# Kernel optimization log

Measured on AMD Instinct MI355X. Metric: run time of the kernel, lower is better.

Reference implementation:

```python
import jax, jax.numpy as jnp
import numpy as np

EPS = 1e-5  # torch BatchNorm1d default eps


def _bn(y2d, g, b):
    # BatchNorm1d in training mode: biased batch stats over axis 0
    m = y2d.mean(axis=0)
    v = y2d.var(axis=0)
    return (y2d - m) * jax.lax.rsqrt(v + EPS) * g + b


def setup_inputs() -> dict:
    key = jax.random.key(0)
    ks = jax.random.split(key, 18)
    S, B, D, H, O = 1000, 64, 440, 512, 1000
    u = lambda k, shape, n: jax.random.uniform(k, shape, jnp.float32, -1.0 / np.sqrt(n), 1.0 / np.sqrt(n))
    fin = np.sqrt(0.01 / (H + O))
    return {
        "x": jax.random.normal(ks[0], (S, B, D), jnp.float32),
        "Wh": u(ks[1], (H, D), D),
        "Wz": u(ks[2], (H, D), D),
        "Wr": u(ks[3], (H, D), D),
        "Uh": u(ks[4], (H, H), H),
        "Uz": u(ks[5], (H, H), H),
        "Ur": u(ks[6], (H, H), H),
        "gh": 1.0 + 0.1 * jax.random.normal(ks[7], (H,), jnp.float32),
        "bh": 0.1 * jax.random.normal(ks[8], (H,), jnp.float32),
        "gz": 1.0 + 0.1 * jax.random.normal(ks[9], (H,), jnp.float32),
        "bz": 0.1 * jax.random.normal(ks[10], (H,), jnp.float32),
        "gr": 1.0 + 0.1 * jax.random.normal(ks[11], (H,), jnp.float32),
        "br": 0.1 * jax.random.normal(ks[12], (H,), jnp.float32),
        "Wf": jax.random.uniform(ks[13], (O, H), jnp.float32, -fin, fin),
        "gf": 1.0 + 0.1 * jax.random.normal(ks[14], (O,), jnp.float32),
        "bf": 0.1 * jax.random.normal(ks[15], (O,), jnp.float32),
    }


def reference(x, Wh, Wz, Wr, Uh, Uz, Ur, gh, bh, gz, bz, gr, br, Wf, gf, bf):
    S, B, D = x.shape
    H = Wh.shape[0]
    xf = x.reshape(S * B, D)
    # gate input projections (no bias; BN in train mode over flattened (S*B, H))
    wh = _bn(xf @ Wh.T, gh, bh).reshape(S, B, H)
    wz = _bn(xf @ Wz.T, gz, bz).reshape(S, B, H)
    wr = _bn(xf @ Wr.T, gr, br).reshape(S, B, H)

    def step(ht, gates):
        whk, wzk, wrk = gates
        zt = jax.nn.sigmoid(wzk + ht @ Uz.T)
        rt = jax.nn.sigmoid(wrk + ht @ Ur.T)
        hcand = jnp.tanh(whk + (rt * ht) @ Uh.T)  # drop_mask==1 (gru_drop=0.0)
        ht = zt * ht + (1.0 - zt) * hcand
        return ht, ht

    h0 = jnp.zeros((B, H), x.dtype)
    _, h = jax.lax.scan(step, h0, (wh, wz, wr))  # h: (S, B, H)

    ws = _bn(h.reshape(S * B, H) @ Wf.T, gf, bf)
    return jax.nn.log_softmax(ws, axis=1)
```

## Files before the change

### kernel.cpp

```cpp
#include <hip/hip_runtime.h>
#include <cstdint>

typedef unsigned short u16;
typedef unsigned long long u64;
typedef __attribute__((ext_vector_type(8))) short bf16x8;
typedef __attribute__((ext_vector_type(4))) float f32x4;

#define S_LEN 1000
#define NWG   32

#define OFF_HALL   0ull
#define SZ_HALL    (1001ull*64*512*2)
#define OFF_WCAT   (OFF_HALL + SZ_HALL)
#define SZ_WCAT    (1536ull*448*2)
#define OFF_WFB    (OFF_WCAT + SZ_WCAT)
#define SZ_WFB     (1024ull*512*2)
#define OFF_RH     (OFF_WFB + SZ_WFB)
#define SZ_RH      (64ull*512*2)
#define OFF_GSUM   (OFF_RH + SZ_RH)
#define OFF_GSQ    (OFF_GSUM + 1536*4)
#define OFF_AALL   (OFF_GSQ  + 1536*4)
#define OFF_CALL   (OFF_AALL + 1536*4)
#define OFF_SSUM   (OFF_CALL + 1536*4)
#define OFF_SSQ    (OFF_SSUM + 1024*4)
#define OFF_AF     (OFF_SSQ  + 1024*4)
#define OFF_CF     (OFF_AF   + 1024*4)
#define OFF_FLAGS  (OFF_CF   + 1024*4)
#define STATS_ZERO_BYTES (OFF_FLAGS + 2048 - OFF_SSUM)

__device__ __forceinline__ float bf2f(u16 u) {
  union { unsigned u; float f; } v; v.u = ((unsigned)u) << 16; return v.f;
}
__device__ __forceinline__ u16 f2bf(float f) {
  union { float f; unsigned u; } v; v.f = f;
  unsigned r = (v.u + 0x7fffu + ((v.u >> 16) & 1u)) >> 16;
  return (u16)r;
}
__device__ __forceinline__ float sigm(float x) { return 1.f / (1.f + __expf(-x)); }
__device__ __forceinline__ float tanh_(float x) {
  float e = __expf(-2.f * fabsf(x));
  float r = (1.f - e) / (1.f + e);
  return x >= 0.f ? r : -r;
}

__device__ __forceinline__ u64 ld8(const u16* p) {
  return __hip_atomic_load((const u64*)p, __ATOMIC_RELAXED, __HIP_MEMORY_SCOPE_AGENT);
}
__device__ __forceinline__ void st4(u16* p, unsigned v) {
  __hip_atomic_store((unsigned*)p, v, __ATOMIC_RELAXED, __HIP_MEMORY_SCOPE_AGENT);
}
union Frag { u64 q[2]; bf16x8 v; };

__device__ __forceinline__ void stage16(const u16* g, u16* l) {
  __builtin_amdgcn_global_load_lds((const __attribute__((address_space(1))) unsigned int*)(g),
                                   (__attribute__((address_space(3))) unsigned int*)(l), 16, 0, 0);
}

__global__ void cvt_pad(const float* __restrict__ src, u16* __restrict__ dst, int incols, int outcols) {
  int r = blockIdx.x, ci = threadIdx.x;
  float v = (ci < incols) ? src[(size_t)r * incols + ci] : 0.f;
  dst[(size_t)r * outcols + ci] = f2bf(v);
}
__global__ void cvt_wf(const float* __restrict__ src, u16* __restrict__ dst) {
  int r = blockIdx.x, ci = threadIdx.x;
  float v = (r < 1000) ? src[(size_t)r * 512 + ci] : 0.f;
  dst[(size_t)r * 512 + ci] = f2bf(v);
}

template<int MODE>
__global__ __launch_bounds__(256, 1) void gemm_bt(const u16* __restrict__ A, const u16* __restrict__ B,
                                                  void* __restrict__ Cout, int K, int ldc, int nlimit) {
  __shared__ __align__(16) u16 smem[16 * 512];
  const int bm = blockIdx.x * 128;
  const int bn = blockIdx.y * 128;
  const int tid = threadIdx.x;
  const int w = tid >> 6;
  const int lane = tid & 63;
  const int r = lane & 15;
  const int q = lane >> 4;
  const int wm = w & 1, wn = w >> 1;

  f32x4 acc[4][4];
#pragma unroll
  for (int i = 0; i < 4; ++i)
#pragma unroll
    for (int j = 0; j < 4; ++j) acc[i][j] = (f32x4){0.f, 0.f, 0.f, 0.f};

  const u16* gA0 = A + (size_t)(bm + w * 16 + r) * K + q * 8;
  const u16* gA1 = A + (size_t)(bm + (w + 4) * 16 + r) * K + q * 8;
  const u16* gB0 = B + (size_t)(bn + w * 16 + r) * K + q * 8;
  const u16* gB1 = B + (size_t)(bn + (w + 4) * 16 + r) * K + q * 8;
  u16* As = smem;
  u16* Bs = smem + 8 * 512;

  for (int k0 = 0; k0 < K; k0 += 32) {
    stage16(gA0 + k0, As + w * 512);
    stage16(gA1 + k0, As + (w + 4) * 512);
    stage16(gB0 + k0, Bs + w * 512);
    stage16(gB1 + k0, Bs + (w + 4) * 512);
    __syncthreads();
    bf16x8 af[4], bf_[4];
#pragma unroll
    for (int mi = 0; mi < 4; ++mi) af[mi] = *(const bf16x8*)(As + (wm * 4 + mi) * 512 + lane * 8);
#pragma unroll
    for (int ni = 0; ni < 4; ++ni) bf_[ni] = *(const bf16x8*)(Bs + (wn * 4 + ni) * 512 + lane * 8);
#pragma unroll
    for (int mi = 0; mi < 4; ++mi)
#pragma unroll
      for (int ni = 0; ni < 4; ++ni)
        acc[mi][ni] = __builtin_amdgcn_mfma_f32_16x16x32_bf16(af[mi], bf_[ni], acc[mi][ni], 0, 0, 0);
    __syncthreads();
  }
  const int row0 = bm + wm * 64;
  const int col0 = bn + wn * 64;
#pragma unroll
  for (int mi = 0; mi < 4; ++mi)
#pragma unroll
    for (int ni = 0; ni < 4; ++ni) {
      int cc = col0 + ni * 16 + r;
      int rr = row0 + mi * 16 + q * 4;
      if (MODE == 1) {
#pragma unroll
        for (int i = 0; i < 4; ++i)
          if (cc < nlimit) ((float*)Cout)[(size_t)(rr + i) * ldc + cc] = acc[mi][ni][i];
      } else {
        u64 pk = (u64)f2bf(acc[mi][ni][0]) | ((u64)f2bf(acc[mi][ni][1]) << 16) |
                 ((u64)f2bf(acc[mi][ni][2]) << 32) | ((u64)f2bf(acc[mi][ni][3]) << 48);
        *(u64*)((u16*)Cout + (size_t)cc * ldc + rr) = pk;
      }
    }
}

__global__ __launch_bounds__(256, 1) void rowstats(const u16* __restrict__ G,
                                                   float* __restrict__ sum, float* __restrict__ sumsq) {
  const int n = blockIdx.x;
  const u16* row = G + (size_t)n * 64000;
  float s = 0.f, ss = 0.f;
  for (int idx = threadIdx.x * 8; idx < 64000; idx += 2048) {
    union { bf16x8 v; u16 e[8]; } u;
    u.v = *(const bf16x8*)(row + idx);
#pragma unroll
    for (int e = 0; e < 8; ++e) { float f = bf2f(u.e[e]); s += f; ss += f * f; }
  }
#pragma unroll
  for (int o = 32; o > 0; o >>= 1) { s += __shfl_xor(s, o); ss += __shfl_xor(ss, o); }
  __shared__ float ls[4], lss[4];
  if ((threadIdx.x & 63) == 0) { ls[threadIdx.x >> 6] = s; lss[threadIdx.x >> 6] = ss; }
  __syncthreads();
  if (threadIdx.x == 0) {
    sum[n]   = ls[0] + ls[1] + ls[2] + ls[3];
    sumsq[n] = lss[0] + lss[1] + lss[2] + lss[3];
  }
}

__global__ __launch_bounds__(256, 1) void colstats_f32(const float* __restrict__ X, int ld, int ncols,
                                                       float* __restrict__ sum, float* __restrict__ sumsq) {
  const int col = blockIdx.x * 128 + (threadIdx.x & 127);
  const int half = threadIdx.x >> 7;
  const int r0 = blockIdx.y * 2000;
  float s = 0.f, ss = 0.f;
  if (col < ncols) {
    for (int rr = r0 + half; rr < r0 + 2000; rr += 2) {
      float v = X[(size_t)rr * ld + col]; s += v; ss += v * v;
    }
  }
  __shared__ float ls[128], lss[128];
  if (half) { ls[threadIdx.x & 127] = s; lss[threadIdx.x & 127] = ss; }
  __syncthreads();
  if (!half && col < ncols) {
    s += ls[threadIdx.x]; ss += lss[threadIdx.x];
    atomicAdd(&sum[col], s); atomicAdd(&sumsq[col], ss);
  }
}

__global__ void fin_gate(const float* __restrict__ sum, const float* __restrict__ sq,
                         const float* gh, const float* bh, const float* gz, const float* bz,
                         const float* gr, const float* br, float* __restrict__ a, float* __restrict__ c) {
  int j = blockIdx.x * 256 + threadIdx.x;
  if (j >= 1536) return;
  float m = sum[j] * (1.f / 64000.f);
  float v = sq[j] * (1.f / 64000.f) - m * m;
  int seg = j >> 9, jj = j & 511;
  float gg = seg == 0 ? gh[jj] : seg == 1 ? gz[jj] : gr[jj];
  float bb = seg == 0 ? bh[jj] : seg == 1 ? bz[jj] : br[jj];
  float aa = gg * rsqrtf(v + 1e-5f);
  a[j] = aa; c[j] = bb - m * aa;
}

__global__ void fin_score(const float* __restrict__ sum, const float* __restrict__ sq,
                          const float* __restrict__ gfp, const float* __restrict__ bfp,
                          float* __restrict__ a, float* __restrict__ c) {
  int j = blockIdx.x * 256 + threadIdx.x;
  if (j >= 1000) return;
  float m = sum[j] * (1.f / 64000.f);
  float v = sq[j] * (1.f / 64000.f) - m * m;
  float aa = gfp[j] * rsqrtf(v + 1e-5f);
  a[j] = aa; c[j] = bfp[j] - m * aa;
}

__device__ __forceinline__ void publish_and_wait(unsigned* flags, int g, unsigned val) {
  asm volatile("s_waitcnt vmcnt(0)" ::: "memory");
  __syncthreads();
  if (threadIdx.x == 0)
    __hip_atomic_store(&flags[g * 16], val, __ATOMIC_RELAXED, __HIP_MEMORY_SCOPE_AGENT);
  if (threadIdx.x < 64) {
    const int l = threadIdx.x;
    for (;;) {
      unsigned v = (l < NWG) ? __hip_atomic_load(&flags[l * 16], __ATOMIC_RELAXED, __HIP_MEMORY_SCOPE_AGENT)
                             : val;
      if (__all(v >= val)) break;
      __builtin_amdgcn_s_sleep(1);
    }
  }
  __syncthreads();
  asm volatile("" ::: "memory");
}

__global__ __launch_bounds__(256, 1) void scan_kernel(
    const u16* __restrict__ gatesT,
    const float* __restrict__ Uz, const float* __restrict__ Ur, const float* __restrict__ Uh,
    const float* __restrict__ acoef, const float* __restrict__ ccoef,
    u16* __restrict__ hall,
    u16* __restrict__ rh,
    unsigned* __restrict__ flags) {
  __shared__ __align__(16) u16 Us[3][16][520];
  __shared__ float co[6][16];
  const int g = blockIdx.x;
  const int j0 = g * 16;
  const int tid = threadIdx.x;
  const int w = tid >> 6;
  const int lane = tid & 63;
  const int r = lane & 15;
  const int q = lane >> 4;

  for (int idx = tid; idx < 3 * 16 * 512; idx += 256) {
    int u = idx >> 13;
    int rem = idx & 8191;
    int j = rem >> 9;
    int k = rem & 511;
    const float* U = (u == 0) ? Uz : (u == 1) ? Ur : Uh;
    Us[u][j][k] = f2bf(U[(size_t)(j0 + j) * 512 + k]);
  }
  if (tid < 16) {
    co[0][tid] = acoef[512 + j0 + tid];  co[1][tid] = ccoef[512 + j0 + tid];
    co[2][tid] = acoef[1024 + j0 + tid]; co[3][tid] = ccoef[1024 + j0 + tid];
    co[4][tid] = acoef[j0 + tid];        co[5][tid] = ccoef[j0 + tid];
  }
  __syncthreads();
  const float az = co[0][r], cz = co[1][r], ar = co[2][r], cr = co[3][r];
  const float ah = co[4][r], ch = co[5][r];

  const u16* gRowH = gatesT + (size_t)(j0 + r) * 64000;
  const u16* gRowZ = gatesT + (size_t)(512 + j0 + r) * 64000;
  const u16* gRowR = gatesT + (size_t)(1024 + j0 + r) * 64000;

  float hp[4] = {0.f, 0.f, 0.f, 0.f};

  for (int t = 1; t <= S_LEN; ++t) {
    const int ct = (t - 1) * 64 + w * 16 + q * 4;
    const u64 wzq = *(const u64*)(gRowZ + ct);
    const u64 wrq = *(const u64*)(gRowR + ct);
    const u64 whq = *(const u64*)(gRowH + ct);

    const u16* hprev = hall + (size_t)(t - 1) * (64 * 512);
    f32x4 accz = {0.f, 0.f, 0.f, 0.f}, accr = {0.f, 0.f, 0.f, 0.f};
    const u16* arow = hprev + (size_t)(w * 16 + r) * 512 + q * 8;
#pragma unroll
    for (int ks = 0; ks < 16; ++ks) {
      Frag a; a.q[0] = ld8(arow + ks * 32); a.q[1] = ld8(arow + ks * 32 + 4);
      bf16x8 bz = *(const bf16x8*)(&Us[0][r][ks * 32 + q * 8]);
      bf16x8 br2 = *(const bf16x8*)(&Us[1][r][ks * 32 + q * 8]);
      accz = __builtin_amdgcn_mfma_f32_16x16x32_bf16(a.v, bz, accz, 0, 0, 0);
      accr = __builtin_amdgcn_mfma_f32_16x16x32_bf16(a.v, br2, accr, 0, 0, 0);
    }
    float zv[4];
#pragma unroll
    for (int i = 0; i < 4; ++i) {
      float wz = bf2f((u16)(wzq >> (16 * i)));
      float wr = bf2f((u16)(wrq >> (16 * i)));
      zv[i] = sigm(accz[i] + wz * az + cz);
      float rv = sigm(accr[i] + wr * ar + cr);
      u16 rhb = f2bf(rv * hp[i]);
      float partner = __shfl_xor(bf2f(rhb), 1);
      if ((r & 1) == 0)
        st4(rh + (size_t)(w * 16 + q * 4 + i) * 512 + j0 + r,
            (unsigned)rhb | ((unsigned)f2bf(partner) << 16));
    }
    publish_and_wait(flags, g, 2 * t - 1);

    f32x4 acch = {0.f, 0.f, 0.f, 0.f};
    const u16* rrow = rh + (size_t)(w * 16 + r) * 512 + q * 8;
#pragma unroll
    for (int ks = 0; ks < 16; ++ks) {
      Frag a; a.q[0] = ld8(rrow + ks * 32); a.q[1] = ld8(rrow + ks * 32 + 4);
      bf16x8 bh = *(const bf16x8*)(&Us[2][r][ks * 32 + q * 8]);
      acch = __builtin_amdgcn_mfma_f32_16x16x32_bf16(a.v, bh, acch, 0, 0, 0);
    }
    u16* hnew = hall + (size_t)t * (64 * 512);
#pragma unroll
    for (int i = 0; i < 4; ++i) {
      float wh = bf2f((u16)(whq >> (16 * i)));
      float hc = tanh_(acch[i] + wh * ah + ch);
      float hn = zv[i] * hp[i] + (1.f - zv[i]) * hc;
      u16 hb = f2bf(hn);
      hp[i] = bf2f(hb);
      float partner = __shfl_xor(hp[i], 1);
      if ((r & 1) == 0)
        st4(hnew + (size_t)(w * 16 + q * 4 + i) * 512 + j0 + r,
            (unsigned)hb | ((unsigned)f2bf(partner) << 16));
    }
    publish_and_wait(flags, g, 2 * t);
  }
}

__global__ __launch_bounds__(256, 1) void logsoftmax_k(float* __restrict__ S,
                                                       const float* __restrict__ a, const float* __restrict__ c) {
  __shared__ float as_[1000], cs_[1000];
  for (int i = threadIdx.x; i < 1000; i += 256) { as_[i] = a[i]; cs_[i] = c[i]; }
  __syncthreads();
  const int w = threadIdx.x >> 6, lane = threadIdx.x & 63;
  for (int it = 0; it < 4; ++it) {
    const int row = blockIdx.x * 16 + it * 4 + w;
    float* Srow = S + (size_t)row * 1000;
    float tv[16];
    float mx = -3.0e38f;
#pragma unroll
    for (int qq = 0; qq < 16; ++qq) {
      int j = lane + qq * 64;
      float v = -3.0e38f;
      if (j < 1000) v = as_[j] * Srow[j] + cs_[j];
      tv[qq] = v;
      mx = fmaxf(mx, v);
    }
#pragma unroll
    for (int o = 32; o > 0; o >>= 1) mx = fmaxf(mx, __shfl_xor(mx, o));
    float sm = 0.f;
#pragma unroll
    for (int qq = 0; qq < 16; ++qq) sm += __expf(tv[qq] - mx);
#pragma unroll
    for (int o = 32; o > 0; o >>= 1) sm += __shfl_xor(sm, o);
    float lse = mx + __logf(sm);
#pragma unroll
    for (int qq = 0; qq < 16; ++qq) {
      int j = lane + qq * 64;
      if (j < 1000) Srow[j] = tv[qq] - lse;
    }
  }
}

extern "C" void kernel_launch(void* const* d_in, const int* in_sizes, int n_in,
                              void* d_out, int out_size, void* d_ws, size_t ws_size,
                              hipStream_t stream) {
  const float* x  = (const float*)d_in[0];
  const float* Wh = (const float*)d_in[1];
  const float* Wz = (const float*)d_in[2];
  const float* Wr = (const float*)d_in[3];
  const float* Uh = (const float*)d_in[4];
  const float* Uz = (const float*)d_in[5];
  const float* Ur = (const float*)d_in[6];
  const float* gh = (const float*)d_in[7];
  const float* bh = (const float*)d_in[8];
  const float* gz = (const float*)d_in[9];
  const float* bz = (const float*)d_in[10];
  const float* gr = (const float*)d_in[11];
  const float* br = (const float*)d_in[12];
  const float* Wf = (const float*)d_in[13];
  const float* gf = (const float*)d_in[14];
  const float* bfp = (const float*)d_in[15];

  uint8_t* ws = (uint8_t*)d_ws;
  u16* hall = (u16*)(ws + OFF_HALL);
  u16* xb   = (u16*)(ws + OFF_HALL);
  u16* wcat = (u16*)(ws + OFF_WCAT);
  u16* wfb  = (u16*)(ws + OFF_WFB);
  u16* rh   = (u16*)(ws + OFF_RH);
  float* gsum = (float*)(ws + OFF_GSUM);
  float* gsq  = (float*)(ws + OFF_GSQ);
  float* aall = (float*)(ws + OFF_AALL);
  float* call = (float*)(ws + OFF_CALL);
  float* ssum = (float*)(ws + OFF_SSUM);
  float* ssq  = (float*)(ws + OFF_SSQ);
  float* af   = (float*)(ws + OFF_AF);
  float* cf   = (float*)(ws + OFF_CF);
  unsigned* flags = (unsigned*)(ws + OFF_FLAGS);

  u16* gatesT = (u16*)d_out;
  float* scores = (float*)d_out;

  hipMemsetAsync(ws + OFF_SSUM, 0, (size_t)STATS_ZERO_BYTES, stream);

  cvt_pad<<<dim3(64000), dim3(448), 0, stream>>>(x, xb, 440, 448);
  cvt_pad<<<dim3(512), dim3(448), 0, stream>>>(Wh, wcat, 440, 448);
  cvt_pad<<<dim3(512), dim3(448), 0, stream>>>(Wz, wcat + 512 * 448, 440, 448);
  cvt_pad<<<dim3(512), dim3(448), 0, stream>>>(Wr, wcat + 1024 * 448, 440, 448);
  cvt_wf<<<dim3(1024), dim3(512), 0, stream>>>(Wf, wfb);

  gemm_bt<2><<<dim3(500, 12), dim3(256), 0, stream>>>(xb, wcat, (void*)gatesT, 448, 64000, 1536);

  rowstats<<<dim3(1536), dim3(256), 0, stream>>>(gatesT, gsum, gsq);
  fin_gate<<<dim3(6), dim3(256), 0, stream>>>(gsum, gsq, gh, bh, gz, bz, gr, br, aall, call);

  hipMemsetAsync(ws + OFF_HALL, 0, (size_t)(64 * 512 * 2), stream);

  scan_kernel<<<dim3(NWG), dim3(256), 0, stream>>>(gatesT, Uz, Ur, Uh, aall, call, hall, rh, flags);

  gemm_bt<1><<<dim3(500, 8), dim3(256), 0, stream>>>(hall + 64 * 512, wfb, (void*)scores, 512, 1000, 1000);

  colstats_f32<<<dim3(8, 32), dim3(256), 0, stream>>>(scores, 1000, 1000, ssum, ssq);
  fin_score<<<dim3(4), dim3(256), 0, stream>>>(ssum, ssq, gf, bfp, af, cf);

  logsoftmax_k<<<dim3(4000), dim3(256), 0, stream>>>(scores, af, cf);
}
```

Baseline: 12.63 ms.

## Replace flag barriers in GRU scan with step-tagged data words

The two grid-wide flag barriers per timestep in the persistent scan kernel are removed. Each bf16 value of h and r*h is now written as a 32-bit word whose high half carries the timestep tag, into double-buffered exchange arrays. Consumers spin-read the operands, check every tag, and redo the MFMA accumulation until all tags match. This cuts the barrier round-trip latency, but each load now moves twice the bytes, the unpack adds ALU work, and whole accumulations may be recomputed on retry.

```diff
diff --git a/kernel.cpp b/kernel.cpp
--- a/kernel.cpp
+++ b/kernel.cpp
@@ -2,6 +2,7 @@
 #include <cstdint>
 
 typedef unsigned short u16;
+typedef unsigned u32;
 typedef unsigned long long u64;
 typedef __attribute__((ext_vector_type(8))) short bf16x8;
 typedef __attribute__((ext_vector_type(4))) float f32x4;
@@ -13,11 +14,13 @@
 #define SZ_HALL    (1001ull*64*512*2)
 #define OFF_WCAT   (OFF_HALL + SZ_HALL)
 #define SZ_WCAT    (1536ull*448*2)
+#define OFF_HX     (OFF_WCAT)
+#define SZ_HX      (2ull*64*512*4)
+#define OFF_RHX    (OFF_HX + SZ_HX)
+#define SZ_RHX     (2ull*64*512*4)
 #define OFF_WFB    (OFF_WCAT + SZ_WCAT)
 #define SZ_WFB     (1024ull*512*2)
-#define OFF_RH     (OFF_WFB + SZ_WFB)
-#define SZ_RH      (64ull*512*2)
-#define OFF_GSUM   (OFF_RH + SZ_RH)
+#define OFF_GSUM   (OFF_WFB + SZ_WFB)
 #define OFF_GSQ    (OFF_GSUM + 1536*4)
 #define OFF_AALL   (OFF_GSQ  + 1536*4)
 #define OFF_CALL   (OFF_AALL + 1536*4)
@@ -25,8 +28,9 @@
 #define OFF_SSQ    (OFF_SSUM + 1024*4)
 #define OFF_AF     (OFF_SSQ  + 1024*4)
 #define OFF_CF     (OFF_AF   + 1024*4)
-#define OFF_FLAGS  (OFF_CF   + 1024*4)
-#define STATS_ZERO_BYTES (OFF_FLAGS + 2048 - OFF_SSUM)
+#define STATS_ZERO_BYTES (OFF_CF + 1024*4 - OFF_SSUM)
+
+#define TAGMASK 0xFFFF0000FFFF0000ull
 
 __device__ __forceinline__ float bf2f(u16 u) {
   union { unsigned u; float f; } v; v.u = ((unsigned)u) << 16; return v.f;
@@ -43,13 +47,12 @@
   return x >= 0.f ? r : -r;
 }
 
-__device__ __forceinline__ u64 ld8(const u16* p) {
+__device__ __forceinline__ u64 ld8(const u32* p) {
   return __hip_atomic_load((const u64*)p, __ATOMIC_RELAXED, __HIP_MEMORY_SCOPE_AGENT);
 }
-__device__ __forceinline__ void st4(u16* p, unsigned v) {
-  __hip_atomic_store((unsigned*)p, v, __ATOMIC_RELAXED, __HIP_MEMORY_SCOPE_AGENT);
-}
-union Frag { u64 q[2]; bf16x8 v; };
+__device__ __forceinline__ void st4(u32* p, u32 v) {
+  __hip_atomic_store(p, v, __ATOMIC_RELAXED, __HIP_MEMORY_SCOPE_AGENT);
+}
 
 __device__ __forceinline__ void stage16(const u16* g, u16* l) {
   __builtin_amdgcn_global_load_lds((const __attribute__((address_space(1))) unsigned int*)(g),
@@ -198,31 +201,13 @@
   a[j] = aa; c[j] = bfp[j] - m * aa;
 }
 
-__device__ __forceinline__ void publish_and_wait(unsigned* flags, int g, unsigned val) {
-  asm volatile("s_waitcnt vmcnt(0)" ::: "memory");
-  __syncthreads();
-  if (threadIdx.x == 0)
-    __hip_atomic_store(&flags[g * 16], val, __ATOMIC_RELAXED, __HIP_MEMORY_SCOPE_AGENT);
-  if (threadIdx.x < 64) {
-    const int l = threadIdx.x;
-    for (;;) {
-      unsigned v = (l < NWG) ? __hip_atomic_load(&flags[l * 16], __ATOMIC_RELAXED, __HIP_MEMORY_SCOPE_AGENT)
-                             : val;
-      if (__all(v >= val)) break;
-      __builtin_amdgcn_s_sleep(1);
-    }
-  }
-  __syncthreads();
-  asm volatile("" ::: "memory");
-}
-
 __global__ __launch_bounds__(256, 1) void scan_kernel(
     const u16* __restrict__ gatesT,
     const float* __restrict__ Uz, const float* __restrict__ Ur, const float* __restrict__ Uh,
     const float* __restrict__ acoef, const float* __restrict__ ccoef,
     u16* __restrict__ hall,
-    u16* __restrict__ rh,
-    unsigned* __restrict__ flags) {
+    u32* __restrict__ hx,
+    u32* __restrict__ rhx) {
   __shared__ __align__(16) u16 Us[3][16][520];
   __shared__ float co[6][16];
   const int g = blockIdx.x;
@@ -254,6 +239,9 @@
   const u16* gRowZ = gatesT + (size_t)(512 + j0 + r) * 64000;
   const u16* gRowR = gatesT + (size_t)(1024 + j0 + r) * 64000;
 
+  const int arow_off = (w * 16 + r) * 512 + q * 8;
+  const int prow0 = (w * 16 + q * 4) * 512 + j0 + r;
+
   float hp[4] = {0.f, 0.f, 0.f, 0.f};
 
   for (int t = 1; t <= S_LEN; ++t) {
@@ -262,17 +250,37 @@
     const u64 wrq = *(const u64*)(gRowR + ct);
     const u64 whq = *(const u64*)(gRowH + ct);
 
-    const u16* hprev = hall + (size_t)(t - 1) * (64 * 512);
-    f32x4 accz = {0.f, 0.f, 0.f, 0.f}, accr = {0.f, 0.f, 0.f, 0.f};
-    const u16* arow = hprev + (size_t)(w * 16 + r) * 512 + q * 8;
-#pragma unroll
-    for (int ks = 0; ks < 16; ++ks) {
-      Frag a; a.q[0] = ld8(arow + ks * 32); a.q[1] = ld8(arow + ks * 32 + 4);
-      bf16x8 bz = *(const bf16x8*)(&Us[0][r][ks * 32 + q * 8]);
-      bf16x8 br2 = *(const bf16x8*)(&Us[1][r][ks * 32 + q * 8]);
-      accz = __builtin_amdgcn_mfma_f32_16x16x32_bf16(a.v, bz, accz, 0, 0, 0);
-      accr = __builtin_amdgcn_mfma_f32_16x16x32_bf16(a.v, br2, accr, 0, 0, 0);
-    }
+    const u32* hsrc = hx + (size_t)((t - 1) & 1) * (64 * 512) + arow_off;
+    const u32 tgA = (u32)(t - 1) << 16;
+    const u64 expA = (u64)tgA | ((u64)tgA << 32);
+    f32x4 accz, accr;
+    for (;;) {
+      accz = (f32x4){0.f, 0.f, 0.f, 0.f};
+      accr = (f32x4){0.f, 0.f, 0.f, 0.f};
+      u64 bad = 0;
+#pragma unroll
+      for (int ks = 0; ks < 16; ++ks) {
+        u64 a0 = ld8(hsrc + ks * 32);
+        u64 a1 = ld8(hsrc + ks * 32 + 2);
+        u64 a2 = ld8(hsrc + ks * 32 + 4);
+        u64 a3 = ld8(hsrc + ks * 32 + 6);
+        bad |= (a0 ^ expA) | (a1 ^ expA);
+        bad |= (a2 ^ expA) | (a3 ^ expA);
+        union { u32 p[4]; bf16x8 v; } f;
+        f.p[0] = ((u32)a0 & 0xFFFFu) | ((u32)(a0 >> 32) << 16);
+        f.p[1] = ((u32)a1 & 0xFFFFu) | ((u32)(a1 >> 32) << 16);
+        f.p[2] = ((u32)a2 & 0xFFFFu) | ((u32)(a2 >> 32) << 16);
+        f.p[3] = ((u32)a3 & 0xFFFFu) | ((u32)(a3 >> 32) << 16);
+        bf16x8 bz = *(const bf16x8*)(&Us[0][r][ks * 32 + q * 8]);
+        bf16x8 br2 = *(const bf16x8*)(&Us[1][r][ks * 32 + q * 8]);
+        accz = __builtin_amdgcn_mfma_f32_16x16x32_bf16(f.v, bz, accz, 0, 0, 0);
+        accr = __builtin_amdgcn_mfma_f32_16x16x32_bf16(f.v, br2, accr, 0, 0, 0);
+      }
+      if (__all((bad & TAGMASK) == 0ull)) break;
+      __builtin_amdgcn_s_sleep(2);
+    }
+    const u32 tgT = (u32)t << 16;
+    u32* rdst = rhx + (size_t)(t & 1) * (64 * 512) + prow0;
     float zv[4];
 #pragma unroll
     for (int i = 0; i < 4; ++i) {
@@ -280,23 +288,36 @@
       float wr = bf2f((u16)(wrq >> (16 * i)));
       zv[i] = sigm(accz[i] + wz * az + cz);
       float rv = sigm(accr[i] + wr * ar + cr);
-      u16 rhb = f2bf(rv * hp[i]);
-      float partner = __shfl_xor(bf2f(rhb), 1);
-      if ((r & 1) == 0)
-        st4(rh + (size_t)(w * 16 + q * 4 + i) * 512 + j0 + r,
-            (unsigned)rhb | ((unsigned)f2bf(partner) << 16));
-    }
-    publish_and_wait(flags, g, 2 * t - 1);
-
-    f32x4 acch = {0.f, 0.f, 0.f, 0.f};
-    const u16* rrow = rh + (size_t)(w * 16 + r) * 512 + q * 8;
-#pragma unroll
-    for (int ks = 0; ks < 16; ++ks) {
-      Frag a; a.q[0] = ld8(rrow + ks * 32); a.q[1] = ld8(rrow + ks * 32 + 4);
-      bf16x8 bh = *(const bf16x8*)(&Us[2][r][ks * 32 + q * 8]);
-      acch = __builtin_amdgcn_mfma_f32_16x16x32_bf16(a.v, bh, acch, 0, 0, 0);
-    }
-    u16* hnew = hall + (size_t)t * (64 * 512);
+      st4(rdst + i * 512, tgT | (u32)f2bf(rv * hp[i]));
+    }
+
+    const u32* rsrc = rhx + (size_t)(t & 1) * (64 * 512) + arow_off;
+    const u64 expB = (u64)tgT | ((u64)tgT << 32);
+    f32x4 acch;
+    for (;;) {
+      acch = (f32x4){0.f, 0.f, 0.f, 0.f};
+      u64 bad = 0;
+#pragma unroll
+      for (int ks = 0; ks < 16; ++ks) {
+        u64 a0 = ld8(rsrc + ks * 32);
+        u64 a1 = ld8(rsrc + ks * 32 + 2);
+        u64 a2 = ld8(rsrc + ks * 32 + 4);
+        u64 a3 = ld8(rsrc + ks * 32 + 6);
+        bad |= (a0 ^ expB) | (a1 ^ expB);
+        bad |= (a2 ^ expB) | (a3 ^ expB);
+        union { u32 p[4]; bf16x8 v; } f;
+        f.p[0] = ((u32)a0 & 0xFFFFu) | ((u32)(a0 >> 32) << 16);
+        f.p[1] = ((u32)a1 & 0xFFFFu) | ((u32)(a1 >> 32) << 16);
+        f.p[2] = ((u32)a2 & 0xFFFFu) | ((u32)(a2 >> 32) << 16);
+        f.p[3] = ((u32)a3 & 0xFFFFu) | ((u32)(a3 >> 32) << 16);
+        bf16x8 bh = *(const bf16x8*)(&Us[2][r][ks * 32 + q * 8]);
+        acch = __builtin_amdgcn_mfma_f32_16x16x32_bf16(f.v, bh, acch, 0, 0, 0);
+      }
+      if (__all((bad & TAGMASK) == 0ull)) break;
+      __builtin_amdgcn_s_sleep(2);
+    }
+    u16* hrow = hall + (size_t)t * (64 * 512);
+    u32* hdst = hx + (size_t)(t & 1) * (64 * 512) + prow0;
 #pragma unroll
     for (int i = 0; i < 4; ++i) {
       float wh = bf2f((u16)(whq >> (16 * i)));
@@ -304,12 +325,9 @@
       float hn = zv[i] * hp[i] + (1.f - zv[i]) * hc;
       u16 hb = f2bf(hn);
       hp[i] = bf2f(hb);
-      float partner = __shfl_xor(hp[i], 1);
-      if ((r & 1) == 0)
-        st4(hnew + (size_t)(w * 16 + q * 4 + i) * 512 + j0 + r,
-            (unsigned)hb | ((unsigned)f2bf(partner) << 16));
-    }
-    publish_and_wait(flags, g, 2 * t);
+      hrow[(size_t)(w * 16 + q * 4 + i) * 512 + j0 + r] = hb;
+      st4(hdst + i * 512, tgT | (u32)hb);
+    }
   }
 }
 
@@ -373,7 +391,8 @@
   u16* xb   = (u16*)(ws + OFF_HALL);
   u16* wcat = (u16*)(ws + OFF_WCAT);
   u16* wfb  = (u16*)(ws + OFF_WFB);
-  u16* rh   = (u16*)(ws + OFF_RH);
+  u32* hx   = (u32*)(ws + OFF_HX);
+  u32* rhx  = (u32*)(ws + OFF_RHX);
   float* gsum = (float*)(ws + OFF_GSUM);
   float* gsq  = (float*)(ws + OFF_GSQ);
   float* aall = (float*)(ws + OFF_AALL);
@@ -382,7 +401,6 @@
   float* ssq  = (float*)(ws + OFF_SSQ);
   float* af   = (float*)(ws + OFF_AF);
   float* cf   = (float*)(ws + OFF_CF);
-  unsigned* flags = (unsigned*)(ws + OFF_FLAGS);
 
   u16* gatesT = (u16*)d_out;
   float* scores = (float*)d_out;
@@ -400,9 +418,9 @@
   rowstats<<<dim3(1536), dim3(256), 0, stream>>>(gatesT, gsum, gsq);
   fin_gate<<<dim3(6), dim3(256), 0, stream>>>(gsum, gsq, gh, bh, gz, bz, gr, br, aall, call);
 
-  hipMemsetAsync(ws + OFF_HALL, 0, (size_t)(64 * 512 * 2), stream);
-
-  scan_kernel<<<dim3(NWG), dim3(256), 0, stream>>>(gatesT, Uz, Ur, Uh, aall, call, hall, rh, flags);
+  hipMemsetAsync(ws + OFF_HX, 0, (size_t)(SZ_HX + SZ_RHX), stream);
+
+  scan_kernel<<<dim3(NWG), dim3(256), 0, stream>>>(gatesT, Uz, Ur, Uh, aall, call, hall, hx, rhx);
 
   gemm_bt<1><<<dim3(500, 8), dim3(256), 0, stream>>>(hall + 64 * 512, wfb, (void*)scores, 512, 1000, 1000);
 
```

Result: slower. 35.11 ms (+178.0%).

## Split recurrent scan by batch across workgroups to eliminate inter-workgroup barriers

Applied to the files above, without the earlier changes.

The GRU scan now partitions the batch into four independent 16-row groups instead of splitting the hidden dimension across 32 workgroups. Each workgroup computes the full hidden state for its rows, so the two global flag barriers per timestep are gone and h and r*h are exchanged through LDS with __syncthreads. The recurrent U matrices are converted to bf16 once by a new kernel into spare output memory and streamed from global/L2 every step. This removes the grid-wide synchronisation latency, but it leaves only four CUs active and each step re-reads roughly 1.5MB of weights per workgroup.

```diff
diff --git a/kernel.cpp b/kernel.cpp
--- a/kernel.cpp
+++ b/kernel.cpp
@@ -2,12 +2,12 @@
 #include <cstdint>
 
 typedef unsigned short u16;
+typedef unsigned u32;
 typedef unsigned long long u64;
 typedef __attribute__((ext_vector_type(8))) short bf16x8;
 typedef __attribute__((ext_vector_type(4))) float f32x4;
 
 #define S_LEN 1000
-#define NWG   32
 
 #define OFF_HALL   0ull
 #define SZ_HALL    (1001ull*64*512*2)
@@ -15,9 +15,7 @@
 #define SZ_WCAT    (1536ull*448*2)
 #define OFF_WFB    (OFF_WCAT + SZ_WCAT)
 #define SZ_WFB     (1024ull*512*2)
-#define OFF_RH     (OFF_WFB + SZ_WFB)
-#define SZ_RH      (64ull*512*2)
-#define OFF_GSUM   (OFF_RH + SZ_RH)
+#define OFF_GSUM   (OFF_WFB + SZ_WFB)
 #define OFF_GSQ    (OFF_GSUM + 1536*4)
 #define OFF_AALL   (OFF_GSQ  + 1536*4)
 #define OFF_CALL   (OFF_AALL + 1536*4)
@@ -25,8 +23,7 @@
 #define OFF_SSQ    (OFF_SSUM + 1024*4)
 #define OFF_AF     (OFF_SSQ  + 1024*4)
 #define OFF_CF     (OFF_AF   + 1024*4)
-#define OFF_FLAGS  (OFF_CF   + 1024*4)
-#define STATS_ZERO_BYTES (OFF_FLAGS + 2048 - OFF_SSUM)
+#define STATS_ZERO_BYTES (OFF_CF + 1024*4 - OFF_SSUM)
 
 __device__ __forceinline__ float bf2f(u16 u) {
   union { unsigned u; float f; } v; v.u = ((unsigned)u) << 16; return v.f;
@@ -43,14 +40,6 @@
   return x >= 0.f ? r : -r;
 }
 
-__device__ __forceinline__ u64 ld8(const u16* p) {
-  return __hip_atomic_load((const u64*)p, __ATOMIC_RELAXED, __HIP_MEMORY_SCOPE_AGENT);
-}
-__device__ __forceinline__ void st4(u16* p, unsigned v) {
-  __hip_atomic_store((unsigned*)p, v, __ATOMIC_RELAXED, __HIP_MEMORY_SCOPE_AGENT);
-}
-union Frag { u64 q[2]; bf16x8 v; };
-
 __device__ __forceinline__ void stage16(const u16* g, u16* l) {
   __builtin_amdgcn_global_load_lds((const __attribute__((address_space(1))) unsigned int*)(g),
                                    (__attribute__((address_space(3))) unsigned int*)(l), 16, 0, 0);
@@ -65,6 +54,14 @@
   int r = blockIdx.x, ci = threadIdx.x;
   float v = (r < 1000) ? src[(size_t)r * 512 + ci] : 0.f;
   dst[(size_t)r * 512 + ci] = f2bf(v);
+}
+__global__ void cvt_u(const float* __restrict__ Uz, const float* __restrict__ Ur,
+                      const float* __restrict__ Uh, u16* __restrict__ dst) {
+  const int m = blockIdx.y;
+  const int row = blockIdx.x;
+  const int c = threadIdx.x;
+  const float* src = m == 0 ? Uz : m == 1 ? Ur : Uh;
+  dst[((size_t)m * 512 + row) * 512 + c] = f2bf(src[(size_t)row * 512 + c]);
 }
 
 template<int MODE>
@@ -198,118 +195,144 @@
   a[j] = aa; c[j] = bfp[j] - m * aa;
 }
 
-__device__ __forceinline__ void publish_and_wait(unsigned* flags, int g, unsigned val) {
-  asm volatile("s_waitcnt vmcnt(0)" ::: "memory");
-  __syncthreads();
-  if (threadIdx.x == 0)
-    __hip_atomic_store(&flags[g * 16], val, __ATOMIC_RELAXED, __HIP_MEMORY_SCOPE_AGENT);
-  if (threadIdx.x < 64) {
-    const int l = threadIdx.x;
-    for (;;) {
-      unsigned v = (l < NWG) ? __hip_atomic_load(&flags[l * 16], __ATOMIC_RELAXED, __HIP_MEMORY_SCOPE_AGENT)
-                             : val;
-      if (__all(v >= val)) break;
-      __builtin_amdgcn_s_sleep(1);
-    }
-  }
-  __syncthreads();
-  asm volatile("" ::: "memory");
-}
-
 __global__ __launch_bounds__(256, 1) void scan_kernel(
     const u16* __restrict__ gatesT,
-    const float* __restrict__ Uz, const float* __restrict__ Ur, const float* __restrict__ Uh,
+    const u16* __restrict__ Ub,
     const float* __restrict__ acoef, const float* __restrict__ ccoef,
-    u16* __restrict__ hall,
-    u16* __restrict__ rh,
-    unsigned* __restrict__ flags) {
-  __shared__ __align__(16) u16 Us[3][16][520];
-  __shared__ float co[6][16];
-  const int g = blockIdx.x;
-  const int j0 = g * 16;
+    u16* __restrict__ hall) {
+  __shared__ __align__(16) u16 h_buf[16][520];
+  __shared__ __align__(16) u16 rh_buf[16][520];
+  const int grp = blockIdx.x;
   const int tid = threadIdx.x;
   const int w = tid >> 6;
   const int lane = tid & 63;
   const int r = lane & 15;
   const int q = lane >> 4;
-
-  for (int idx = tid; idx < 3 * 16 * 512; idx += 256) {
-    int u = idx >> 13;
-    int rem = idx & 8191;
-    int j = rem >> 9;
-    int k = rem & 511;
-    const float* U = (u == 0) ? Uz : (u == 1) ? Ur : Uh;
-    Us[u][j][k] = f2bf(U[(size_t)(j0 + j) * 512 + k]);
-  }
-  if (tid < 16) {
-    co[0][tid] = acoef[512 + j0 + tid];  co[1][tid] = ccoef[512 + j0 + tid];
-    co[2][tid] = acoef[1024 + j0 + tid]; co[3][tid] = ccoef[1024 + j0 + tid];
-    co[4][tid] = acoef[j0 + tid];        co[5][tid] = ccoef[j0 + tid];
-  }
+  const int jw = w * 128;
+
+  for (int idx = tid; idx < 16 * 520 / 2; idx += 256) ((u32*)h_buf)[idx] = 0;
+
+  float caz[8], ccz[8], car[8], ccr[8], cah[8], cch[8];
+#pragma unroll
+  for (int n = 0; n < 8; ++n) {
+    int j = jw + n * 16 + r;
+    caz[n] = acoef[512 + j];  ccz[n] = ccoef[512 + j];
+    car[n] = acoef[1024 + j]; ccr[n] = ccoef[1024 + j];
+    cah[n] = acoef[j];        cch[n] = ccoef[j];
+  }
+  const u16* Uzb = Ub;
+  const u16* Urb = Ub + 512 * 512;
+  const u16* Uhb = Ub + 2 * 512 * 512;
+  const u16* gH = gatesT + (size_t)(jw + r) * 64000 + grp * 16 + q * 4;
+  const u16* gZ = gatesT + (size_t)(512 + jw + r) * 64000 + grp * 16 + q * 4;
+  const u16* gR = gatesT + (size_t)(1024 + jw + r) * 64000 + grp * 16 + q * 4;
+
+  float hp[8][4];
+#pragma unroll
+  for (int n = 0; n < 8; ++n)
+#pragma unroll
+    for (int i = 0; i < 4; ++i) hp[n][i] = 0.f;
+
   __syncthreads();
-  const float az = co[0][r], cz = co[1][r], ar = co[2][r], cr = co[3][r];
-  const float ah = co[4][r], ch = co[5][r];
-
-  const u16* gRowH = gatesT + (size_t)(j0 + r) * 64000;
-  const u16* gRowZ = gatesT + (size_t)(512 + j0 + r) * 64000;
-  const u16* gRowR = gatesT + (size_t)(1024 + j0 + r) * 64000;
-
-  float hp[4] = {0.f, 0.f, 0.f, 0.f};
 
   for (int t = 1; t <= S_LEN; ++t) {
-    const int ct = (t - 1) * 64 + w * 16 + q * 4;
-    const u64 wzq = *(const u64*)(gRowZ + ct);
-    const u64 wrq = *(const u64*)(gRowR + ct);
-    const u64 whq = *(const u64*)(gRowH + ct);
-
-    const u16* hprev = hall + (size_t)(t - 1) * (64 * 512);
-    f32x4 accz = {0.f, 0.f, 0.f, 0.f}, accr = {0.f, 0.f, 0.f, 0.f};
-    const u16* arow = hprev + (size_t)(w * 16 + r) * 512 + q * 8;
-#pragma unroll
-    for (int ks = 0; ks < 16; ++ks) {
-      Frag a; a.q[0] = ld8(arow + ks * 32); a.q[1] = ld8(arow + ks * 32 + 4);
-      bf16x8 bz = *(const bf16x8*)(&Us[0][r][ks * 32 + q * 8]);
-      bf16x8 br2 = *(const bf16x8*)(&Us[1][r][ks * 32 + q * 8]);
-      accz = __builtin_amdgcn_mfma_f32_16x16x32_bf16(a.v, bz, accz, 0, 0, 0);
-      accr = __builtin_amdgcn_mfma_f32_16x16x32_bf16(a.v, br2, accr, 0, 0, 0);
-    }
-    float zv[4];
-#pragma unroll
-    for (int i = 0; i < 4; ++i) {
-      float wz = bf2f((u16)(wzq >> (16 * i)));
-      float wr = bf2f((u16)(wrq >> (16 * i)));
-      zv[i] = sigm(accz[i] + wz * az + cz);
-      float rv = sigm(accr[i] + wr * ar + cr);
-      u16 rhb = f2bf(rv * hp[i]);
-      float partner = __shfl_xor(bf2f(rhb), 1);
-      if ((r & 1) == 0)
-        st4(rh + (size_t)(w * 16 + q * 4 + i) * 512 + j0 + r,
-            (unsigned)rhb | ((unsigned)f2bf(partner) << 16));
-    }
-    publish_and_wait(flags, g, 2 * t - 1);
-
-    f32x4 acch = {0.f, 0.f, 0.f, 0.f};
-    const u16* rrow = rh + (size_t)(w * 16 + r) * 512 + q * 8;
-#pragma unroll
-    for (int ks = 0; ks < 16; ++ks) {
-      Frag a; a.q[0] = ld8(rrow + ks * 32); a.q[1] = ld8(rrow + ks * 32 + 4);
-      bf16x8 bh = *(const bf16x8*)(&Us[2][r][ks * 32 + q * 8]);
-      acch = __builtin_amdgcn_mfma_f32_16x16x32_bf16(a.v, bh, acch, 0, 0, 0);
-    }
-    u16* hnew = hall + (size_t)t * (64 * 512);
-#pragma unroll
-    for (int i = 0; i < 4; ++i) {
-      float wh = bf2f((u16)(whq >> (16 * i)));
-      float hc = tanh_(acch[i] + wh * ah + ch);
-      float hn = zv[i] * hp[i] + (1.f - zv[i]) * hc;
-      u16 hb = f2bf(hn);
-      hp[i] = bf2f(hb);
-      float partner = __shfl_xor(hp[i], 1);
-      if ((r & 1) == 0)
-        st4(hnew + (size_t)(w * 16 + q * 4 + i) * 512 + j0 + r,
-            (unsigned)hb | ((unsigned)f2bf(partner) << 16));
-    }
-    publish_and_wait(flags, g, 2 * t);
+    const size_t tof = (size_t)(t - 1) * 64;
+    u64 wzq[8], wrq[8], whq[8];
+#pragma unroll
+    for (int n = 0; n < 8; ++n) {
+      wzq[n] = *(const u64*)(gZ + (size_t)n * (16 * 64000) + tof);
+      wrq[n] = *(const u64*)(gR + (size_t)n * (16 * 64000) + tof);
+      whq[n] = *(const u64*)(gH + (size_t)n * (16 * 64000) + tof);
+    }
+    bf16x8 ah[16];
+#pragma unroll
+    for (int ks = 0; ks < 16; ++ks)
+      ah[ks] = *(const bf16x8*)(&h_buf[r][ks * 32 + q * 8]);
+
+    f32x4 accz[8], accr[8];
+#pragma unroll
+    for (int n = 0; n < 8; ++n) { accz[n] = (f32x4){0.f,0.f,0.f,0.f}; accr[n] = (f32x4){0.f,0.f,0.f,0.f}; }
+#pragma unroll
+    for (int n = 0; n < 8; ++n) {
+      const u16* bzp = Uzb + (size_t)(jw + n * 16 + r) * 512 + q * 8;
+      const u16* brp = Urb + (size_t)(jw + n * 16 + r) * 512 + q * 8;
+      bf16x8 bz[16], br[16];
+#pragma unroll
+      for (int ks = 0; ks < 16; ++ks) {
+        bz[ks] = *(const bf16x8*)(bzp + ks * 32);
+        br[ks] = *(const bf16x8*)(brp + ks * 32);
+      }
+#pragma unroll
+      for (int ks = 0; ks < 16; ++ks) {
+        accz[n] = __builtin_amdgcn_mfma_f32_16x16x32_bf16(ah[ks], bz[ks], accz[n], 0, 0, 0);
+        accr[n] = __builtin_amdgcn_mfma_f32_16x16x32_bf16(ah[ks], br[ks], accr[n], 0, 0, 0);
+      }
+    }
+    float zvv[8][4];
+#pragma unroll
+    for (int n = 0; n < 8; ++n) {
+      const int j = jw + n * 16 + r;
+#pragma unroll
+      for (int i = 0; i < 4; ++i) {
+        float wr_ = bf2f((u16)(wrq[n] >> (16 * i)));
+        float rv = sigm(accr[n][i] + wr_ * car[n] + ccr[n]);
+        u16 rhb = f2bf(rv * hp[n][i]);
+        float partner = __shfl_xor(bf2f(rhb), 1);
+        if ((r & 1) == 0)
+          *(u32*)(&rh_buf[q * 4 + i][j]) = (u32)rhb | ((u32)f2bf(partner) << 16);
+        float wz_ = bf2f((u16)(wzq[n] >> (16 * i)));
+        zvv[n][i] = sigm(accz[n][i] + wz_ * caz[n] + ccz[n]);
+      }
+    }
+    __syncthreads();
+
+    bf16x8 a2[16];
+#pragma unroll
+    for (int ks = 0; ks < 16; ++ks)
+      a2[ks] = *(const bf16x8*)(&rh_buf[r][ks * 32 + q * 8]);
+    f32x4 acch[8];
+#pragma unroll
+    for (int n = 0; n < 8; ++n) acch[n] = (f32x4){0.f,0.f,0.f,0.f};
+#pragma unroll
+    for (int np = 0; np < 8; np += 2) {
+      const u16* b0p = Uhb + (size_t)(jw + np * 16 + r) * 512 + q * 8;
+      const u16* b1p = b0p + 16 * 512;
+      bf16x8 b0[16], b1[16];
+#pragma unroll
+      for (int ks = 0; ks < 16; ++ks) {
+        b0[ks] = *(const bf16x8*)(b0p + ks * 32);
+        b1[ks] = *(const bf16x8*)(b1p + ks * 32);
+      }
+#pragma unroll
+      for (int ks = 0; ks < 16; ++ks) {
+        acch[np]     = __builtin_amdgcn_mfma_f32_16x16x32_bf16(a2[ks], b0[ks], acch[np], 0, 0, 0);
+        acch[np + 1] = __builtin_amdgcn_mfma_f32_16x16x32_bf16(a2[ks], b1[ks], acch[np + 1], 0, 0, 0);
+      }
+    }
+#pragma unroll
+    for (int n = 0; n < 8; ++n) {
+      const int j = jw + n * 16 + r;
+#pragma unroll
+      for (int i = 0; i < 4; ++i) {
+        float wh_ = bf2f((u16)(whq[n] >> (16 * i)));
+        float hc = tanh_(acch[n][i] + wh_ * cah[n] + cch[n]);
+        float hn = zvv[n][i] * hp[n][i] + (1.f - zvv[n][i]) * hc;
+        u16 hb = f2bf(hn);
+        hp[n][i] = bf2f(hb);
+        float partner = __shfl_xor(bf2f(hb), 1);
+        if ((r & 1) == 0)
+          *(u32*)(&h_buf[q * 4 + i][j]) = (u32)hb | ((u32)f2bf(partner) << 16);
+      }
+    }
+    __syncthreads();
+
+    u16* hrow = hall + (size_t)(t * 64 + grp * 16) * 512;
+#pragma unroll
+    for (int it = 0; it < 4; ++it) {
+      const int row = it * 4 + w;
+      bf16x8 v = *(const bf16x8*)(&h_buf[row][lane * 8]);
+      *(bf16x8*)(hrow + (size_t)row * 512 + lane * 8) = v;
+    }
   }
 }
 
@@ -373,7 +396,6 @@
   u16* xb   = (u16*)(ws + OFF_HALL);
   u16* wcat = (u16*)(ws + OFF_WCAT);
   u16* wfb  = (u16*)(ws + OFF_WFB);
-  u16* rh   = (u16*)(ws + OFF_RH);
   float* gsum = (float*)(ws + OFF_GSUM);
   float* gsq  = (float*)(ws + OFF_GSQ);
   float* aall = (float*)(ws + OFF_AALL);
@@ -382,9 +404,9 @@
   float* ssq  = (float*)(ws + OFF_SSQ);
   float* af   = (float*)(ws + OFF_AF);
   float* cf   = (float*)(ws + OFF_CF);
-  unsigned* flags = (unsigned*)(ws + OFF_FLAGS);
 
   u16* gatesT = (u16*)d_out;
+  u16* Ub = (u16*)d_out + (size_t)1536 * 64000;
   float* scores = (float*)d_out;
 
   hipMemsetAsync(ws + OFF_SSUM, 0, (size_t)STATS_ZERO_BYTES, stream);
@@ -394,15 +416,14 @@
   cvt_pad<<<dim3(512), dim3(448), 0, stream>>>(Wz, wcat + 512 * 448, 440, 448);
   cvt_pad<<<dim3(512), dim3(448), 0, stream>>>(Wr, wcat + 1024 * 448, 440, 448);
   cvt_wf<<<dim3(1024), dim3(512), 0, stream>>>(Wf, wfb);
+  cvt_u<<<dim3(512, 3), dim3(512), 0, stream>>>(Uz, Ur, Uh, Ub);
 
   gemm_bt<2><<<dim3(500, 12), dim3(256), 0, stream>>>(xb, wcat, (void*)gatesT, 448, 64000, 1536);
 
   rowstats<<<dim3(1536), dim3(256), 0, stream>>>(gatesT, gsum, gsq);
   fin_gate<<<dim3(6), dim3(256), 0, stream>>>(gsum, gsq, gh, bh, gz, bz, gr, br, aall, call);
 
-  hipMemsetAsync(ws + OFF_HALL, 0, (size_t)(64 * 512 * 2), stream);
-
-  scan_kernel<<<dim3(NWG), dim3(256), 0, stream>>>(gatesT, Uz, Ur, Uh, aall, call, hall, rh, flags);
+  scan_kernel<<<dim3(4), dim3(256), 0, stream>>>(gatesT, Ub, aall, call, hall);
 
   gemm_bt<1><<<dim3(500, 8), dim3(256), 0, stream>>>(hall + 64 * 512, wfb, (void*)scores, 512, 1000, 1000);
 
```

Result: slower. 48.66 ms (+285.4%).
